# Optimization experiments

Measured on AMD Instinct MI355X. Metric: run time of the kernel, lower is better.

## Reference

```python
import jax, jax.numpy as jnp
import numpy as np

N_QUBITS = 14
N_LAYERS = 3
BATCH = 128


def _apply_1q(state, gate, w, n):
    """Apply a single-qubit gate on wire w (PennyLane wire 0 = most significant bit).
    state: (B, 2**n) complex. gate: (2,2) shared or (B,2,2) batched."""
    L, R = 2 ** w, 2 ** (n - 1 - w)
    s = state.reshape(-1, L, 2, R)
    if gate.ndim == 2:
        s = jnp.einsum('ij,aljr->alir', gate, s)
    else:
        s = jnp.einsum('aij,aljr->alir', gate, s)
    return s.reshape(state.shape)


def _apply_cnot(state, c, t, n):
    """CNOT with control wire c, target wire t on (B, 2**n) state."""
    s = state.reshape((-1,) + (2,) * n)
    ca = 1 + c
    s0 = jax.lax.index_in_dim(s, 0, ca, keepdims=False)
    s1 = jax.lax.index_in_dim(s, 1, ca, keepdims=False)
    # axis of target after removing control axis
    ta = 1 + t if t < c else t
    s1 = jnp.flip(s1, axis=ta)
    return jnp.stack([s0, s1], axis=ca).reshape(state.shape)


def _rx_gates(angles):
    """Batched RX gate matrices. angles: (B,) -> (B,2,2) complex64."""
    half = angles * 0.5
    c = jnp.cos(half).astype(jnp.complex64)
    s = (-1j) * jnp.sin(half).astype(jnp.complex64)
    return jnp.stack([jnp.stack([c, s], -1), jnp.stack([s, c], -1)], -2)


def _rot_gate(phi, theta, omega):
    """PennyLane Rot(phi,theta,omega) = RZ(omega) RY(theta) RZ(phi), (2,2) complex."""
    ct = jnp.cos(theta * 0.5).astype(jnp.complex64)
    st = jnp.sin(theta * 0.5).astype(jnp.complex64)
    ep = jnp.exp(-0.5j * (phi + omega))  # e^{-i(phi+omega)/2}
    em = jnp.exp(-0.5j * (phi - omega))  # e^{-i(phi-omega)/2}
    return jnp.stack([
        jnp.stack([ep * ct, -jnp.conj(em) * st]),
        jnp.stack([em * st, jnp.conj(ep) * ct]),
    ]).astype(jnp.complex64)


def _simulate(x, q_weights):
    B, n = x.shape
    state = jnp.zeros((B, 2 ** n), jnp.complex64).at[:, 0].set(1.0)
    # AngleEmbedding: RX(x_i) on wire i
    for w in range(n):
        state = _apply_1q(state, _rx_gates(x[:, w]), w, n)
    # StronglyEntanglingLayers: Rot on each wire, then ring of CNOTs with range r
    n_layers = q_weights.shape[0]
    for l in range(n_layers):
        for w in range(n):
            g = _rot_gate(q_weights[l, w, 0], q_weights[l, w, 1], q_weights[l, w, 2])
            state = _apply_1q(state, g, w, n)
        r = (l % (n - 1)) + 1  # PennyLane default ranges
        for w in range(n):
            state = _apply_cnot(state, w, (w + r) % n, n)
    return state


def _pauli_z_signs(n):
    idx = np.arange(2 ** n, dtype=np.int64)[:, None]
    shifts = np.arange(n - 1, -1, -1, dtype=np.int64)[None, :]  # wire 0 = MSB
    bits = (idx >> shifts) & 1
    return jnp.asarray(1.0 - 2.0 * bits, dtype=jnp.float32)  # (2**n, n)


def setup_inputs() -> dict:
    key = jax.random.key(0)
    k1, k2, k3, k4 = jax.random.split(key, 4)
    x = jax.random.normal(k1, (BATCH, N_QUBITS), dtype=jnp.float32)
    q_weights = jax.random.normal(k2, (N_LAYERS, N_QUBITS, 3), dtype=jnp.float32) * 0.01
    w_lin = jax.random.normal(k3, (1, N_QUBITS), dtype=jnp.float32) / np.sqrt(N_QUBITS)
    b_lin = jax.random.normal(k4, (1,), dtype=jnp.float32) * 0.01
    return {"x": x, "q_weights": q_weights, "w_lin": w_lin, "b_lin": b_lin}


def reference(x, q_weights, w_lin, b_lin):
    n = x.shape[1]
    state = _simulate(x, q_weights)
    probs = (state.real ** 2 + state.imag ** 2).astype(jnp.float32)  # (B, 2**n)
    expvals = probs @ _pauli_z_signs(n)  # (B, n) = <Z_i>
    logits = expvals @ w_lin.T + b_lin  # (B, 1)
    return logits
```

## Files before the change

kernel.cpp:

```cpp
#include <hip/hip_runtime.h>

#define NQ 14
#define NSTATE (1 << NQ)
#define NL 3
#define NPASS (NL * 4)
#define BT 1024
#define NWAVES (BT / 64)

struct PassP {
    unsigned short R[10];
    unsigned short cmb[16];
    unsigned char gidx[4];
    unsigned char nw;
    unsigned char _pad;
};
struct SimParams {
    PassP pass[NPASS];
    unsigned short ms[NQ];
};

struct C2x2 { float2 m[2][2]; };

__device__ __forceinline__ float2 cmul(float2 a, float2 b) {
    return make_float2(a.x * b.x - a.y * b.y, a.x * b.y + a.y * b.x);
}
__device__ __forceinline__ float2 cmac(float2 acc, float2 a, float2 b) {
    acc.x = fmaf(a.x, b.x, fmaf(-a.y, b.y, acc.x));
    acc.y = fmaf(a.x, b.y, fmaf(a.y, b.x, acc.y));
    return acc;
}

__device__ __forceinline__ C2x2 rot_gate(const float* qp) {
    float phi = qp[0], th = qp[1], om = qp[2];
    float ct, stt; __sincosf(0.5f * th, &stt, &ct);
    float sa, ca; __sincosf(0.5f * (phi + om), &sa, &ca);
    float sb, cb; __sincosf(0.5f * (phi - om), &sb, &cb);
    C2x2 G;
    G.m[0][0] = make_float2(ca * ct, -sa * ct);
    G.m[0][1] = make_float2(-cb * stt, -sb * stt);
    G.m[1][0] = make_float2(cb * stt, -sb * stt);
    G.m[1][1] = make_float2(ca * ct, sa * ct);
    return G;
}

__device__ __forceinline__ C2x2 fuse_rx(C2x2 G, float ang) {
    float sh, ch; __sincosf(0.5f * ang, &sh, &ch);
    float2 c = make_float2(ch, 0.f), is = make_float2(0.f, -sh);
    C2x2 R;
    #pragma unroll
    for (int i = 0; i < 2; ++i) {
        R.m[i][0] = cmac(cmul(G.m[i][0], c), G.m[i][1], is);
        R.m[i][1] = cmac(cmul(G.m[i][1], c), G.m[i][0], is);
    }
    return R;
}

__global__ __launch_bounds__(BT) void qsim_kernel(
    const float* __restrict__ x, const float* __restrict__ qw,
    const float* __restrict__ wl, const float* __restrict__ bl,
    float* __restrict__ out, SimParams P)
{
    __shared__ float2 st[NSTATE];
    __shared__ float2 gbuf[NL * NQ * 4];
    __shared__ float red[NWAVES];

    const int tid = threadIdx.x;
    const int b = blockIdx.x;

    for (int t = tid; t < NSTATE; t += BT) st[t] = make_float2(0.f, 0.f);
    if (tid == 0) st[0] = make_float2(1.f, 0.f);

    if (tid < NL * NQ) {
        int l = tid / NQ, w = tid % NQ;
        C2x2 G = rot_gate(qw + tid * 3);
        if (l == 0) G = fuse_rx(G, x[b * NQ + w]);
        gbuf[tid * 4 + 0] = G.m[0][0];
        gbuf[tid * 4 + 1] = G.m[0][1];
        gbuf[tid * 4 + 2] = G.m[1][0];
        gbuf[tid * 4 + 3] = G.m[1][1];
    }

    #pragma unroll 1
    for (int ps = 0; ps < NPASS; ++ps) {
        __syncthreads();

        unsigned r = 0;
        #pragma unroll
        for (int j = 0; j < 10; ++j)
            r ^= ((tid >> j) & 1) ? (unsigned)P.pass[ps].R[j] : 0u;
        const unsigned rb = r << 3;

        unsigned c8[16];
        #pragma unroll
        for (int i = 0; i < 16; ++i)
            c8[i] = ((unsigned)P.pass[ps].cmb[i]) << 3;

        char* sb = (char*)st;
        float2 a[16];
        #pragma unroll
        for (int i = 0; i < 16; ++i)
            a[i] = *(const float2*)(sb + (rb ^ c8[i]));

        const int nw = P.pass[ps].nw;
        #pragma unroll
        for (int q = 0; q < 4; ++q) {
            if (q < nw) {
                const int gi = (int)P.pass[ps].gidx[q] * 4;
                float2 g00 = gbuf[gi + 0], g01 = gbuf[gi + 1];
                float2 g10 = gbuf[gi + 2], g11 = gbuf[gi + 3];
                #pragma unroll
                for (int i = 0; i < 16; ++i) {
                    if (!((i >> q) & 1)) {
                        const int i1 = i | (1 << q);
                        float2 a0 = a[i], a1 = a[i1];
                        float2 n0 = cmac(cmul(g00, a0), g01, a1);
                        float2 n1 = cmac(cmul(g10, a0), g11, a1);
                        a[i] = n0; a[i1] = n1;
                    }
                }
            }
        }

        #pragma unroll
        for (int i = 0; i < 16; ++i)
            *(float2*)(sb + (rb ^ c8[i])) = a[i];
    }

    __syncthreads();

    float A[16];
    #pragma unroll
    for (int k = 0; k < 16; ++k) A[k] = 0.f;
    #pragma unroll
    for (int w = 0; w < NQ; ++w) {
        const unsigned msw = (unsigned)P.ms[w];
        float v = wl[w];
        unsigned s0 = __popc((unsigned)tid & (msw & 1023u)) & 1u;
        float vs = s0 ? -v : v;
        const unsigned hk = msw >> 10;
        #pragma unroll
        for (int k = 0; k < 16; ++k) {
            bool neg = (__popc((unsigned)k & hk) & 1) != 0;
            A[k] += neg ? -vs : vs;
        }
    }

    float acc = 0.f;
    #pragma unroll
    for (int k = 0; k < 16; ++k) {
        float2 a = st[k * BT + tid];
        acc = fmaf(fmaf(a.x, a.x, a.y * a.y), A[k], acc);
    }

    #pragma unroll
    for (int off = 32; off > 0; off >>= 1) acc += __shfl_down(acc, off, 64);
    int lane = tid & 63, wid = tid >> 6;
    if (lane == 0) red[wid] = acc;
    __syncthreads();
    if (tid == 0) {
        float s = 0.f;
        #pragma unroll
        for (int i = 0; i < NWAVES; ++i) s += red[i];
        out[b] = s + bl[0];
    }
}

struct GF2Basis {
    unsigned piv[NQ];
    GF2Basis() { for (int i = 0; i < NQ; ++i) piv[i] = 0; }
    bool insert(unsigned v) {
        for (int bb = NQ - 1; bb >= 0; --bb) {
            if (!((v >> bb) & 1)) continue;
            if (piv[bb]) v ^= piv[bb];
            else { piv[bb] = v; return true; }
        }
        return false;
    }
};

static inline int par16(unsigned v) { return __builtin_parity(v); }
static inline unsigned lcg_next(unsigned& s) { s = s * 1664525u + 1013904223u; return s >> 8; }

static unsigned gf_apply(const unsigned* C, unsigned v) {
    unsigned r = 0;
    while (v) { int j = __builtin_ctz(v); v &= v - 1; r ^= C[j]; }
    return r;
}

static bool gf_invert(const unsigned* C, unsigned* Ci) {
    unsigned rows[NQ], irows[NQ];
    for (int i = 0; i < NQ; ++i) {
        unsigned r = 0;
        for (int j = 0; j < NQ; ++j) r |= ((C[j] >> i) & 1u) << j;
        rows[i] = r; irows[i] = 1u << i;
    }
    for (int c = 0; c < NQ; ++c) {
        int p = -1;
        for (int r = c; r < NQ; ++r) if ((rows[r] >> c) & 1u) { p = r; break; }
        if (p < 0) return false;
        unsigned t = rows[p]; rows[p] = rows[c]; rows[c] = t;
        t = irows[p]; irows[p] = irows[c]; irows[c] = t;
        for (int r = 0; r < NQ; ++r)
            if (r != c && ((rows[r] >> c) & 1u)) { rows[r] ^= rows[c]; irows[r] ^= irows[c]; }
    }
    for (int j = 0; j < NQ; ++j) {
        unsigned col = 0;
        for (int i = 0; i < NQ; ++i) col |= ((irows[i] >> j) & 1u) << i;
        Ci[j] = col;
    }
    return true;
}

extern "C" void kernel_launch(void* const* d_in, const int* in_sizes, int n_in,
                              void* d_out, int out_size, void* d_ws, size_t ws_size,
                              hipStream_t stream) {
    const float* x  = (const float*)d_in[0];
    const float* qw = (const float*)d_in[1];
    const float* wl = (const float*)d_in[2];
    const float* bl = (const float*)d_in[3];
    float* out = (float*)d_out;

    const int B = in_sizes[0] / NQ;

    struct Raw { unsigned mm[4], rv[10], cmb[16]; unsigned char gidx[4], nw; } raw[NPASS];
    unsigned s[NQ], m[NQ], msIdx[NQ];
    for (int w = 0; w < NQ; ++w) s[w] = m[w] = 1u << (NQ - 1 - w);

    int ps = 0;
    for (int l = 0; l < NL; ++l) {
        for (int g0 = 0; g0 < NQ; g0 += 4) {
            int nw = (NQ - g0) < 4 ? (NQ - g0) : 4;
            unsigned mm[4], ss[4];
            GF2Basis gf;
            for (int i = 0; i < nw; ++i) { mm[i] = m[g0 + i]; ss[i] = s[g0 + i]; gf.insert(mm[i]); }
            for (int i = nw; i < 4; ++i) {
                unsigned cand = 0;
                for (int t = 0; t < NQ; ++t)
                    if (gf.insert(1u << t)) { cand = 1u << t; break; }
                for (int j = 0; j < nw; ++j)
                    if (par16(cand & ss[j])) cand ^= mm[j];
                mm[i] = cand; ss[i] = 0;
            }
            int nR = 0;
            for (int t = 0; t < NQ && nR < 10; ++t) {
                if (gf.insert(1u << t)) {
                    unsigned v = 1u << t;
                    for (int j = 0; j < nw; ++j)
                        if (par16(v & ss[j])) v ^= mm[j];
                    raw[ps].rv[nR++] = v;
                }
            }
            for (int idx = 0; idx < 16; ++idx) {
                unsigned c = 0;
                for (int q = 0; q < 4; ++q) if ((idx >> q) & 1) c ^= mm[q];
                raw[ps].cmb[idx] = c;
                if (idx < 4) raw[ps].mm[idx] = mm[idx];
            }
            for (int q = 0; q < 4; ++q)
                raw[ps].gidx[q] = (unsigned char)(q < nw ? (l * NQ + g0 + q) : 0);
            raw[ps].nw = (unsigned char)nw;
            ++ps;
        }
        int r = (l % (NQ - 1)) + 1;
        for (int w = 0; w < NQ; ++w) {
            int c = w, t = (w + r) % NQ;
            s[t] ^= s[c];
            m[c] ^= m[t];
        }
    }
    for (int w = 0; w < NQ; ++w) msIdx[w] = s[w];

    unsigned Cm[NQ], Ci[NQ];
    unsigned seed = 0x9E3779B9u;
    bool found = false;
    for (int tries = 0; tries < 5000 && !found; ++tries) {
        for (int j = 0; j < NQ; ++j) Cm[j] = lcg_next(seed) & (NSTATE - 1);
        if (!gf_invert(Cm, Ci)) continue;
        found = true;
        for (int p = 0; p < NPASS && found; ++p) {
            unsigned piv[4] = {0, 0, 0, 0}; int np = 0;
            for (int i = 0; i < 10; ++i) {
                unsigned w2 = gf_apply(Cm, raw[p].rv[i]);
                for (int bb = 0; bb < 4; ++bb)
                    if (((w2 >> bb) & 1u) && piv[bb]) w2 ^= piv[bb];
                if ((w2 & 15u) && np < 4) { piv[__builtin_ctz(w2 & 15u)] = w2; ++np; }
            }
            if (np < 4) found = false;
        }
    }
    if (!found) {
        for (int j = 0; j < NQ; ++j) Cm[j] = 1u << j;
        gf_invert(Cm, Ci);
    }

    SimParams P;
    for (int p = 0; p < NPASS; ++p) {
        unsigned u[10];
        for (int i = 0; i < 10; ++i) u[i] = gf_apply(Cm, raw[p].rv[i]);
        unsigned piv[4] = {0, 0, 0, 0};
        int ord[10], np = 0, rest[10], nrest = 0;
        for (int i = 0; i < 10; ++i) {
            unsigned w2 = u[i];
            for (int bb = 0; bb < 4; ++bb)
                if (((w2 >> bb) & 1u) && piv[bb]) w2 ^= piv[bb];
            if ((w2 & 15u) && np < 4) { piv[__builtin_ctz(w2 & 15u)] = w2; ord[np++] = i; }
            else rest[nrest++] = i;
        }
        int kk = 0;
        for (int i = 0; i < np; ++i) P.pass[p].R[kk++] = (unsigned short)u[ord[i]];
        for (int i = 0; i < nrest; ++i) P.pass[p].R[kk++] = (unsigned short)u[rest[i]];
        for (int idx = 0; idx < 16; ++idx)
            P.pass[p].cmb[idx] = (unsigned short)gf_apply(Cm, raw[p].cmb[idx]);
        for (int q = 0; q < 4; ++q) P.pass[p].gidx[q] = raw[p].gidx[q];
        P.pass[p].nw = raw[p].nw;
        P.pass[p]._pad = 0;
    }
    for (int w = 0; w < NQ; ++w) {
        unsigned msp = 0;
        for (int i = 0; i < NQ; ++i)
            msp |= (unsigned)(par16(Ci[i] & msIdx[w]) & 1) << i;
        P.ms[w] = (unsigned short)msp;
    }

    qsim_kernel<<<dim3(B), dim3(BT), 0, stream>>>(x, qw, wl, bl, out, P);
}
```

Before: 114.6 us.

## Split Rot gates into diagonal phases and real RY rotations; drop final RZ

For layers after the first, each Rot gate is rewritten as an RZ phase diagonal, a real-valued RY butterfly, and a second RZ diagonal. The per-pass phase tables are precomputed in shared memory. The last layer's omega phases are dropped because they commute through the trailing CNOT permutations and do not change measured probabilities. Gate and phase parameters are now read before the per-pass barrier, and the per-pass metadata is removed from the kernel arguments. The aim is to cut complex FLOPs in the inner butterfly, in exchange for extra phase multiplies and extra register pressure.

```diff
diff --git a/kernel.cpp b/kernel.cpp
--- a/kernel.cpp
+++ b/kernel.cpp
@@ -10,9 +10,6 @@
 struct PassP {
     unsigned short R[10];
     unsigned short cmb[16];
-    unsigned char gidx[4];
-    unsigned char nw;
-    unsigned char _pad;
 };
 struct SimParams {
     PassP pass[NPASS];
@@ -61,7 +58,10 @@
     float* __restrict__ out, SimParams P)
 {
     __shared__ float2 st[NSTATE];
-    __shared__ float2 gbuf[NL * NQ * 4];
+    __shared__ float2 gbuf[16 * 4];
+    __shared__ float2 cs[8 * 4];
+    __shared__ float2 dpre[8][16];
+    __shared__ float2 dpost[4][16];
     __shared__ float red[NWAVES];
 
     const int tid = threadIdx.x;
@@ -70,19 +70,62 @@
     for (int t = tid; t < NSTATE; t += BT) st[t] = make_float2(0.f, 0.f);
     if (tid == 0) st[0] = make_float2(1.f, 0.f);
 
-    if (tid < NL * NQ) {
-        int l = tid / NQ, w = tid % NQ;
-        C2x2 G = rot_gate(qw + tid * 3);
-        if (l == 0) G = fuse_rx(G, x[b * NQ + w]);
+    if (tid < 16) {
+        int p = tid >> 2, q = tid & 3;
+        int nw = (p < 3) ? 4 : 2;
+        C2x2 G;
+        if (q < nw) {
+            int w = p * 4 + q;
+            G = rot_gate(qw + w * 3);
+            G = fuse_rx(G, x[b * NQ + w]);
+        } else {
+            G.m[0][0] = make_float2(1.f, 0.f); G.m[0][1] = make_float2(0.f, 0.f);
+            G.m[1][0] = make_float2(0.f, 0.f); G.m[1][1] = make_float2(1.f, 0.f);
+        }
         gbuf[tid * 4 + 0] = G.m[0][0];
         gbuf[tid * 4 + 1] = G.m[0][1];
         gbuf[tid * 4 + 2] = G.m[1][0];
         gbuf[tid * 4 + 3] = G.m[1][1];
-    }
+    } else if (tid < 48) {
+        int idx = tid - 16, cp = idx >> 2, q = idx & 3;
+        int l = 1 + (cp >> 2), p = cp & 3;
+        int nw = (p < 3) ? 4 : 2;
+        float c = 1.f, s = 0.f;
+        if (q < nw) {
+            float th = qw[(l * NQ + p * 4 + q) * 3 + 1];
+            __sincosf(0.5f * th, &s, &c);
+        }
+        cs[idx] = make_float2(c, s);
+    } else if (tid < 176) {
+        int idx = tid - 48, cp = idx >> 4, i = idx & 15;
+        int l = 1 + (cp >> 2), p = cp & 3;
+        int nw = (p < 3) ? 4 : 2;
+        float ang = 0.f;
+        for (int q = 0; q < nw; ++q) {
+            float ph = 0.5f * qw[(l * NQ + p * 4 + q) * 3 + 0];
+            ang += ((i >> q) & 1) ? ph : -ph;
+        }
+        float sn, cn; __sincosf(ang, &sn, &cn);
+        dpre[cp][i] = make_float2(cn, sn);
+    } else if (tid < 240) {
+        int idx = tid - 176, cp = idx >> 4, i = idx & 15;
+        int p = cp;
+        int nw = (p < 3) ? 4 : 2;
+        float ang = 0.f;
+        for (int q = 0; q < nw; ++q) {
+            float om = 0.5f * qw[(1 * NQ + p * 4 + q) * 3 + 2];
+            ang += ((i >> q) & 1) ? om : -om;
+        }
+        float sn, cn; __sincosf(ang, &sn, &cn);
+        dpost[cp][i] = make_float2(cn, sn);
+    }
+
+    __syncthreads();
 
     #pragma unroll 1
     for (int ps = 0; ps < NPASS; ++ps) {
-        __syncthreads();
+        const int nw = ((ps & 3) < 3) ? 4 : 2;
+        const bool l0 = (ps < 4);
 
         unsigned r = 0;
         #pragma unroll
@@ -95,29 +138,67 @@
         for (int i = 0; i < 16; ++i)
             c8[i] = ((unsigned)P.pass[ps].cmb[i]) << 3;
 
+        float2 g[16]; float2 csr[4]; float2 dp[16];
+        if (l0) {
+            #pragma unroll
+            for (int i = 0; i < 16; ++i) g[i] = gbuf[ps * 16 + i];
+        } else {
+            #pragma unroll
+            for (int q = 0; q < 4; ++q) csr[q] = cs[(ps - 4) * 4 + q];
+            #pragma unroll
+            for (int i = 0; i < 16; ++i) dp[i] = dpre[ps - 4][i];
+        }
+
+        if (ps > 0) __syncthreads();
+
         char* sb = (char*)st;
         float2 a[16];
         #pragma unroll
         for (int i = 0; i < 16; ++i)
             a[i] = *(const float2*)(sb + (rb ^ c8[i]));
 
-        const int nw = P.pass[ps].nw;
-        #pragma unroll
-        for (int q = 0; q < 4; ++q) {
-            if (q < nw) {
-                const int gi = (int)P.pass[ps].gidx[q] * 4;
-                float2 g00 = gbuf[gi + 0], g01 = gbuf[gi + 1];
-                float2 g10 = gbuf[gi + 2], g11 = gbuf[gi + 3];
-                #pragma unroll
-                for (int i = 0; i < 16; ++i) {
-                    if (!((i >> q) & 1)) {
-                        const int i1 = i | (1 << q);
-                        float2 a0 = a[i], a1 = a[i1];
-                        float2 n0 = cmac(cmul(g00, a0), g01, a1);
-                        float2 n1 = cmac(cmul(g10, a0), g11, a1);
-                        a[i] = n0; a[i1] = n1;
+        if (l0) {
+            #pragma unroll
+            for (int q = 0; q < 4; ++q) {
+                if (q < nw) {
+                    float2 g00 = g[q*4+0], g01 = g[q*4+1], g10 = g[q*4+2], g11 = g[q*4+3];
+                    #pragma unroll
+                    for (int i = 0; i < 16; ++i) {
+                        if (!((i >> q) & 1)) {
+                            const int i1 = i | (1 << q);
+                            float2 a0 = a[i], a1 = a[i1];
+                            float2 n0 = cmac(cmul(g00, a0), g01, a1);
+                            float2 n1 = cmac(cmul(g10, a0), g11, a1);
+                            a[i] = n0; a[i1] = n1;
+                        }
                     }
                 }
+            }
+        } else {
+            #pragma unroll
+            for (int i = 0; i < 16; ++i) a[i] = cmul(a[i], dp[i]);
+            #pragma unroll
+            for (int q = 0; q < 4; ++q) {
+                if (q < nw) {
+                    const float c = csr[q].x, s = csr[q].y;
+                    #pragma unroll
+                    for (int i = 0; i < 16; ++i) {
+                        if (!((i >> q) & 1)) {
+                            const int i1 = i | (1 << q);
+                            float2 a0 = a[i], a1 = a[i1];
+                            float2 n0, n1;
+                            n0.x = c * a0.x - s * a1.x;
+                            n0.y = c * a0.y - s * a1.y;
+                            n1.x = s * a0.x + c * a1.x;
+                            n1.y = s * a0.y + c * a1.y;
+                            a[i] = n0; a[i1] = n1;
+                        }
+                    }
+                }
+            }
+            if (ps < 8) {
+                #pragma unroll
+                for (int i = 0; i < 16; ++i) a[i] = cmul(a[i], dpost[ps - 4][i]);
             }
         }
 
@@ -222,7 +303,7 @@
 
     const int B = in_sizes[0] / NQ;
 
-    struct Raw { unsigned mm[4], rv[10], cmb[16]; unsigned char gidx[4], nw; } raw[NPASS];
+    struct Raw { unsigned rv[10], cmb[16]; } raw[NPASS];
     unsigned s[NQ], m[NQ], msIdx[NQ];
     for (int w = 0; w < NQ; ++w) s[w] = m[w] = 1u << (NQ - 1 - w);
 
@@ -254,11 +335,7 @@
                 unsigned c = 0;
                 for (int q = 0; q < 4; ++q) if ((idx >> q) & 1) c ^= mm[q];
                 raw[ps].cmb[idx] = c;
-                if (idx < 4) raw[ps].mm[idx] = mm[idx];
-            }
-            for (int q = 0; q < 4; ++q)
-                raw[ps].gidx[q] = (unsigned char)(q < nw ? (l * NQ + g0 + q) : 0);
-            raw[ps].nw = (unsigned char)nw;
+            }
             ++ps;
         }
         int r = (l % (NQ - 1)) + 1;
@@ -311,9 +388,6 @@
         for (int i = 0; i < nrest; ++i) P.pass[p].R[kk++] = (unsigned short)u[rest[i]];
         for (int idx = 0; idx < 16; ++idx)
             P.pass[p].cmb[idx] = (unsigned short)gf_apply(Cm, raw[p].cmb[idx]);
-        for (int q = 0; q < 4; ++q) P.pass[p].gidx[q] = raw[p].gidx[q];
-        P.pass[p].nw = raw[p].nw;
-        P.pass[p]._pad = 0;
     }
     for (int w = 0; w < NQ; ++w) {
         unsigned msp = 0;
```

Measured after the change: 362.5 us. 216% more time.
